# Kernel optimization log

Hardware: AMD Instinct MI355X
Metric: run time of the kernel (lower is better)

Reference implementation:

```python
import jax, jax.numpy as jnp
import numpy as np

H = 256          # HIDDEN_SIZE
OUT = 3          # output_size (hard-coded SOS input width in the torch code)
N_TO_PREDICT = 64
B, S = 256, 512  # batch, encoder sequence length
IN = H + OUT     # LSTM input size = hidden*D + output_size


def setup_inputs() -> dict:
    key = jax.random.key(0)
    ks = jax.random.split(key, 16)
    sc = 0.05
    return {
        "encoder_outputs": jax.random.normal(ks[0], (B, S, H), jnp.float32),
        "encoder_hidden": jax.random.normal(ks[1], (1, B, H), jnp.float32),
        "encoder_cell": jax.random.normal(ks[2], (1, B, H), jnp.float32),
        # attention params (Va is defined in the torch module but unused in forward)
        "Wa": jax.random.normal(ks[3], (H, H), jnp.float32) * sc,
        "ba": jax.random.normal(ks[4], (H,), jnp.float32) * sc,
        "Ua": jax.random.normal(ks[5], (H, H), jnp.float32) * sc,
        "bua": jax.random.normal(ks[6], (H,), jnp.float32) * sc,
        # single-layer unidirectional LSTM params (torch gate order i,f,g,o)
        "W_ih": jax.random.normal(ks[7], (4 * H, IN), jnp.float32) * sc,
        "W_hh": jax.random.normal(ks[8], (4 * H, H), jnp.float32) * sc,
        "b_ih": jax.random.normal(ks[9], (4 * H,), jnp.float32) * sc,
        "b_hh": jax.random.normal(ks[10], (4 * H,), jnp.float32) * sc,
        # output projection
        "Wo": jax.random.normal(ks[11], (OUT, H), jnp.float32) * sc,
        "bo": jax.random.normal(ks[12], (OUT,), jnp.float32) * sc,
    }


def reference(encoder_outputs, encoder_hidden, encoder_cell,
              Wa, ba, Ua, bua, W_ih, W_hh, b_ih, b_hh, Wo, bo):
    # Precompute Ua(keys): [B,S,H] (same math as recomputing it each step)
    UK = jnp.einsum('bsh,gh->bsg', encoder_outputs, Ua) + bua
    h0 = encoder_hidden[0]  # [B,H] (num_layers=1, unidirectional)
    c0 = encoder_cell[0]
    x0 = jnp.zeros((encoder_outputs.shape[0], OUT), encoder_outputs.dtype)  # SOS_token = 0

    def step(carry, _):
        h, c, x_in = carry
        # Bahdanau-style score as written: Ua(keys) . Wa(query)
        wq = h @ Wa.T + ba                                   # [B,H]
        scores = jnp.einsum('bsh,bh->bs', UK, wq)            # [B,S]
        w = jax.nn.softmax(scores, axis=-1)                  # [B,S]
        ctx = jnp.einsum('bs,bsh->bh', w, encoder_outputs)   # [B,H]
        x = jnp.concatenate([x_in, ctx], axis=-1)            # [B, OUT+H]
        gates = x @ W_ih.T + b_ih + h @ W_hh.T + b_hh        # [B,4H]
        i, f, g, o = jnp.split(gates, 4, axis=-1)
        c_new = jax.nn.sigmoid(f) * c + jax.nn.sigmoid(i) * jnp.tanh(g)
        h_new = jax.nn.sigmoid(o) * jnp.tanh(c_new)
        pred = h_new @ Wo.T + bo                             # [B,OUT]
        return (h_new, c_new, jax.lax.stop_gradient(pred)), (pred, w)

    (hN, cN, _), (preds, attns) = jax.lax.scan(step, (h0, c0, x0), None, length=N_TO_PREDICT)
    predictions = jnp.transpose(preds, (1, 0, 2))   # [B, N, OUT]
    attentions = jnp.transpose(attns, (1, 0, 2))    # [B, N, S]
    decoder_hidden = hN[None]                        # [1, B, H]
    return predictions, decoder_hidden, attentions
```

## Files before the change

kernel.cpp:

```cpp
#include <hip/hip_runtime.h>
#include <math.h>

#define HID   256
#define SEQ   512
#define BATCH 256
#define NPRED 64
#define NOUT  3
#define KP2   264
#define GATES 1024

typedef unsigned int u32;
typedef _Float16 half2_t __attribute__((ext_vector_type(2)));
typedef __fp16   fp16x2_t __attribute__((ext_vector_type(2)));

__device__ __forceinline__ float sigmoidf_(float x) { return 1.0f / (1.0f + __expf(-x)); }
__device__ __forceinline__ float tanhf_(float x)    { return 1.0f - 2.0f / (__expf(2.0f * x) + 1.0f); }

__device__ __forceinline__ float fdot2_(u32 a, u32 b, float c) {
#if __has_builtin(__builtin_amdgcn_fdot2)
    union { u32 u; half2_t h; } x, y; x.u = a; y.u = b;
    return __builtin_amdgcn_fdot2(x.h, y.h, c, false);
#else
    union { u32 u; _Float16 h[2]; } x, y; x.u = a; y.u = b;
    return c + (float)x.h[0] * (float)y.h[0] + (float)x.h[1] * (float)y.h[1];
#endif
}
__device__ __forceinline__ u32 pkrtz_(float a, float b) {
#if __has_builtin(__builtin_amdgcn_cvt_pkrtz)
    union { fp16x2_t h; u32 u; } c; c.h = __builtin_amdgcn_cvt_pkrtz(a, b); return c.u;
#else
    union { _Float16 h[2]; u32 u; } c; c.h[0] = (_Float16)a; c.h[1] = (_Float16)b; return c.u;
#endif
}
__device__ __forceinline__ u32 pkrne_(float a, float b) {
    union { _Float16 h[2]; u32 u; } c; c.h[0] = (_Float16)a; c.h[1] = (_Float16)b; return c.u;
}
__device__ __forceinline__ u32 pkfma_(u32 a, u32 b, u32 c) {
    union { u32 u; half2_t h; } x, y, z, r; x.u = a; y.u = b; z.u = c;
    r.h = x.h * y.h + z.h;
    return r.u;
}
__device__ __forceinline__ u32 pkadd_(u32 a, u32 b) {
    union { u32 u; half2_t h; } x, y, r; x.u = a; y.u = b;
    r.h = x.h + y.h;
    return r.u;
}
__device__ __forceinline__ float lof_(u32 u) {
    union { u32 x; half2_t h; } c; c.x = u; return (float)c.h[0];
}
__device__ __forceinline__ float hif_(u32 u) {
    union { u32 x; half2_t h; } c; c.x = u; return (float)c.h[1];
}

__device__ __forceinline__ float colval_(const float* W_ih, const float* W_hh, int g, int k) {
    if (k < 3)   return W_ih[g * 259 + k];
    if (k == 3)  return 0.f;
    if (k < 260) return W_ih[g * 259 + (k - 1)];
    if (k < 516) return W_hh[g * HID + (k - 260)];
    return 0.f;
}
__global__ void prep_wc(const float* __restrict__ W_ih,
                        const float* __restrict__ W_hh,
                        uint4* __restrict__ Wc2) {
    const int p = blockIdx.x;
    const int j = threadIdx.x;
    u32 comp[4];
    #pragma unroll
    for (int q = 0; q < 4; ++q) {
        const int g = 4 * j + q;
        comp[q] = pkrne_(colval_(W_ih, W_hh, g, 2 * p),
                         colval_(W_ih, W_hh, g, 2 * p + 1));
    }
    Wc2[p * 256 + j] = make_uint4(comp[0], comp[1], comp[2], comp[3]);
}

__global__ void prep_ma(const float* __restrict__ Wa,
                        const float* __restrict__ Ua,
                        uint2* __restrict__ Ma2) {
    const int k4 = blockIdx.x;
    const int j  = threadIdx.x;
    float acc[4] = {0.f, 0.f, 0.f, 0.f};
    for (int m = 0; m < HID; ++m) {
        const float ua = Ua[m * HID + j];
        #pragma unroll
        for (int q = 0; q < 4; ++q)
            acc[q] += Wa[m * HID + 4 * k4 + q] * ua;
    }
    Ma2[k4 * 256 + j] = make_uint2(pkrne_(acc[0], acc[1]), pkrne_(acc[2], acc[3]));
}

__global__ void prep_misc(const float* __restrict__ b_ih,
                          const float* __restrict__ b_hh,
                          const float* __restrict__ ba,
                          const float* __restrict__ Ua,
                          float* __restrict__ bias_g,
                          float* __restrict__ v0) {
    const int t = threadIdx.x;
    if (t < GATES) bias_g[t] = b_ih[t] + b_hh[t];
    if (t < HID) {
        float acc = 0.f;
        for (int m = 0; m < HID; ++m) acc += ba[m] * Ua[m * HID + t];
        v0[t] = acc;
    }
}

__device__ __forceinline__ void p1_body(const uint2* __restrict__ Ma2,
                                        const float* __restrict__ v0,
                                        const u32* s_xh, u32* s_vqh, int j) {
    float a0 = 0.f, a1 = 0.f;
    #pragma unroll 8
    for (int p2 = 0; p2 < 64; ++p2) {
        const uint2 ma = Ma2[(p2 << 8) + j];
        const uint2 hh = *(const uint2*)&s_xh[130 + (p2 << 1)];
        a0 = fdot2_(ma.x, hh.x, a0);
        a1 = fdot2_(ma.y, hh.y, a1);
    }
    float acc = v0[j] + a0 + a1;
    const float accN = __shfl_xor(acc, 1);
    if (!(j & 1)) s_vqh[j >> 1] = pkrtz_(acc, accN);
}

__global__ __launch_bounds__(1024)
void decoder_kernel(const float* __restrict__ enc,
                    const float* __restrict__ h0,
                    const float* __restrict__ c0,
                    const float* __restrict__ Wo,
                    const float* __restrict__ bo,
                    const uint2* __restrict__ Ma2,
                    const float* __restrict__ v0,
                    const uint4* __restrict__ Wc2,
                    const float* __restrict__ bias_g,
                    float* __restrict__ pred_out,
                    float* __restrict__ hid_out,
                    float* __restrict__ attn_out)
{
    const int b    = blockIdx.x;
    const int t    = threadIdx.x;
    const int wave = t >> 6;
    const int lane = t & 63;
    const int rg   = t >> 4;
    const int hc   = t & 15;

    __shared__ __align__(16) float s_h[HID], s_c[HID];
    __shared__ __align__(16) u32   s_vqh[HID / 2];
    __shared__ __align__(16) u32   s_xh[KP2];
    __shared__ __align__(16) float s_gp[4096];
    __shared__ __align__(16) float s_wmax[16], s_wsum[16], s_pred[4];
    u32* const s_gpu = (u32*)s_gp;

    u32 encR[64];
    {
        const float* ep = enc + ((size_t)b * SEQ + rg * 8) * HID + hc * 16;
        #pragma unroll
        for (int rr = 0; rr < 8; ++rr) {
            #pragma unroll
            for (int i2 = 0; i2 < 4; ++i2) {
                const float4 f = *(const float4*)(ep + rr * HID + i2 * 4);
                encR[rr * 8 + i2 * 2]     = pkrne_(f.x, f.y);
                encR[rr * 8 + i2 * 2 + 1] = pkrne_(f.z, f.w);
            }
        }
    }

    if (t < HID) {
        const float hv = h0[b * HID + t];
        s_h[t] = hv;
        s_c[t] = c0[b * HID + t];
        const float hN = __shfl_xor(hv, 1);
        if (!(t & 1)) s_xh[130 + (t >> 1)] = pkrtz_(hv, hN);
    }
    if (t < 2) s_xh[t] = 0u;
    if (t >= 258 && t < KP2) s_xh[t] = 0u;
    if (t < 4) s_pred[t] = 0.f;
    __syncthreads();

    if (t >= 256 && t < 512) p1_body(Ma2, v0, s_xh, s_vqh, t & 255);
    __syncthreads();

    for (int n = 0; n < NPRED; ++n) {
        float acc[8];
        {
            u32 vq[8];
            *(uint4*)&vq[0] = *(const uint4*)&s_vqh[hc * 8];
            *(uint4*)&vq[4] = *(const uint4*)&s_vqh[hc * 8 + 4];
            #pragma unroll
            for (int rr = 0; rr < 8; ++rr) {
                float a = 0.f;
                #pragma unroll
                for (int i = 0; i < 8; ++i) a = fdot2_(encR[rr * 8 + i], vq[i], a);
                acc[rr] = a;
            }
        }
        #pragma unroll
        for (int rr = 0; rr < 8; ++rr) {
            acc[rr] += __shfl_xor(acc[rr], 1);
            acc[rr] += __shfl_xor(acc[rr], 2);
            acc[rr] += __shfl_xor(acc[rr], 4);
            acc[rr] += __shfl_xor(acc[rr], 8);
        }
        float mx = acc[0];
        #pragma unroll
        for (int rr = 1; rr < 8; ++rr) mx = fmaxf(mx, acc[rr]);
        mx = fmaxf(mx, __shfl_xor(mx, 16));
        mx = fmaxf(mx, __shfl_xor(mx, 32));
        if (lane == 0) s_wmax[wave] = mx;
        __syncthreads();

        float M;
        {
            const float4* q4 = (const float4*)s_wmax;
            float4 v = q4[0];
            M = fmaxf(fmaxf(v.x, v.y), fmaxf(v.z, v.w));
            #pragma unroll
            for (int w = 1; w < 4; ++w) {
                v = q4[w];
                M = fmaxf(M, fmaxf(fmaxf(v.x, v.y), fmaxf(v.z, v.w)));
            }
        }
        float e[8];
        #pragma unroll
        for (int rr = 0; rr < 8; ++rr) e[rr] = __expf(acc[rr] - M);
        float su = e[0];
        #pragma unroll
        for (int rr = 1; rr < 8; ++rr) su += e[rr];
        su += __shfl_xor(su, 16);
        su += __shfl_xor(su, 32);
        if (lane == 0) s_wsum[wave] = su;
        __syncthreads();

        float L = 0.f;
        {
            const float4* q4 = (const float4*)s_wsum;
            #pragma unroll
            for (int w = 0; w < 4; ++w) {
                const float4 v = q4[w];
                L += (v.x + v.y) + (v.z + v.w);
            }
        }
        const float invL = 1.0f / L;
        if (hc == 0) {
            float* ap = attn_out + ((size_t)b * NPRED + n) * SEQ + rg * 8;
            float4 o0, o1;
            o0.x = e[0] * invL; o0.y = e[1] * invL; o0.z = e[2] * invL; o0.w = e[3] * invL;
            o1.x = e[4] * invL; o1.y = e[5] * invL; o1.z = e[6] * invL; o1.w = e[7] * invL;
            *(float4*)ap = o0; *(float4*)(ap + 4) = o1;
        }
        u32 wp[8];
        #pragma unroll
        for (int rr = 0; rr < 8; ++rr) {
            const float wn = e[rr] * invL;
            wp[rr] = pkrne_(wn, wn);
        }
        u32 ah[8];
        #pragma unroll
        for (int i = 0; i < 8; ++i) ah[i] = 0u;
        #pragma unroll
        for (int rr = 0; rr < 8; ++rr) {
            #pragma unroll
            for (int i = 0; i < 8; ++i)
                ah[i] = pkfma_(encR[rr * 8 + i], wp[rr], ah[i]);
        }
        #pragma unroll
        for (int i = 0; i < 8; ++i) {
            u32 v = ah[i];
            v = pkadd_(v, (u32)__shfl_xor((int)v, 16));
            v = pkadd_(v, (u32)__shfl_xor((int)v, 32));
            ah[i] = v;
        }
        if ((lane >> 4) == 0) {
            *(uint4*)&s_gpu[wave * 128 + hc * 8]     = *(const uint4*)&ah[0];
            *(uint4*)&s_gpu[wave * 128 + hc * 8 + 4] = *(const uint4*)&ah[4];
        }
        __syncthreads();

        if (t < 128) {
            float cx = 0.f, cy = 0.f;
            #pragma unroll
            for (int w = 0; w < 16; ++w) {
                const u32 u = s_gpu[w * 128 + t];
                cx += lof_(u);
                cy += hif_(u);
            }
            s_xh[2 + t] = pkrne_(cx, cy);
        }
        if (t == 256) {
            s_xh[0] = pkrtz_(s_pred[0], s_pred[1]);
            s_xh[1] = pkrtz_(s_pred[2], 0.f);
        }
        __syncthreads();

        {
            const int j  = t & 255;
            const int ks = t >> 8;
            float4 g4 = {0.f, 0.f, 0.f, 0.f};
            const int pbeg = ks * 66;
            #pragma unroll 3
            for (int pp = 0; pp < 66; ++pp) {
                const int p = pbeg + pp;
                const uint4 w = Wc2[(p << 8) + j];
                const u32 x = s_xh[p];
                g4.x = fdot2_(w.x, x, g4.x);
                g4.y = fdot2_(w.y, x, g4.y);
                g4.z = fdot2_(w.z, x, g4.z);
                g4.w = fdot2_(w.w, x, g4.w);
            }
            *(float4*)&s_gp[(ks << 10) + (j << 2)] = g4;
        }
        __syncthreads();

        if (t < HID) {
            float gv[4];
            #pragma unroll
            for (int q = 0; q < 4; ++q) {
                const int gi = (q << 8) + t;
                gv[q] = bias_g[gi] + s_gp[gi] + s_gp[1024 + gi]
                      + s_gp[2048 + gi] + s_gp[3072 + gi];
            }
            const float cn = sigmoidf_(gv[1]) * s_c[t] + sigmoidf_(gv[0]) * tanhf_(gv[2]);
            const float hn = sigmoidf_(gv[3]) * tanhf_(cn);
            s_c[t] = cn;
            s_h[t] = hn;
            const float hN = __shfl_xor(hn, 1);
            if (!(t & 1)) s_xh[130 + (t >> 1)] = pkrtz_(hn, hN);
        }
        __syncthreads();

        if (wave < NOUT) {
            const float4 w4 = *(const float4*)&Wo[wave * HID + (lane << 2)];
            const float4 h4 = *(const float4*)&s_h[lane << 2];
            float p = w4.x * h4.x + w4.y * h4.y + w4.z * h4.z + w4.w * h4.w;
            #pragma unroll
            for (int off = 32; off >= 1; off >>= 1) p += __shfl_xor(p, off);
            if (lane == 0) {
                p += bo[wave];
                s_pred[wave] = p;
                pred_out[((size_t)b * NPRED + n) * NOUT + wave] = p;
            }
        } else if (t >= 256 && t < 512 && n + 1 < NPRED) {
            p1_body(Ma2, v0, s_xh, s_vqh, t & 255);
        }
        __syncthreads();
    }

    if (t < HID) hid_out[b * HID + t] = s_h[t];
}

extern "C" void kernel_launch(void* const* d_in, const int* in_sizes, int n_in,
                              void* d_out, int out_size, void* d_ws, size_t ws_size,
                              hipStream_t stream) {
    const float* enc  = (const float*)d_in[0];
    const float* h0   = (const float*)d_in[1];
    const float* c0   = (const float*)d_in[2];
    const float* Wa   = (const float*)d_in[3];
    const float* ba   = (const float*)d_in[4];
    const float* Ua   = (const float*)d_in[5];
    const float* W_ih = (const float*)d_in[7];
    const float* W_hh = (const float*)d_in[8];
    const float* b_ih = (const float*)d_in[9];
    const float* b_hh = (const float*)d_in[10];
    const float* Wo   = (const float*)d_in[11];
    const float* bo   = (const float*)d_in[12];

    char* ws = (char*)d_ws;
    uint4* Wc2    = (uint4*)ws;                      ws += (size_t)KP2 * 256 * 16;
    uint2* Ma2    = (uint2*)ws;                      ws += (size_t)64 * 256 * 8;
    float* v0     = (float*)ws;                      ws += 256 * 4;
    float* bias_g = (float*)ws;                      ws += GATES * 4;
    (void)ws_size;

    float* pred_out = (float*)d_out;
    float* hid_out  = pred_out + BATCH * NPRED * NOUT;
    float* attn_out = hid_out + BATCH * HID;

    prep_wc  <<<dim3(KP2), dim3(256),  0, stream>>>(W_ih, W_hh, Wc2);
    prep_ma  <<<dim3(64),  dim3(256),  0, stream>>>(Wa, Ua, Ma2);
    prep_misc<<<dim3(1),   dim3(1024), 0, stream>>>(b_ih, b_hh, ba, Ua, bias_g, v0);
    decoder_kernel<<<dim3(BATCH), dim3(1024), 0, stream>>>(
        enc, h0, c0, Wo, bo, Ma2, v0, Wc2, bias_g,
        pred_out, hid_out, attn_out);
}
```

Before: 1.415 ms.

## Overlap hidden-state gate matvec with prediction phase and defer softmax normalization

```diff
diff --git a/kernel.cpp b/kernel.cpp
--- a/kernel.cpp
+++ b/kernel.cpp
@@ -108,7 +108,7 @@
                                         const float* __restrict__ v0,
                                         const u32* s_xh, u32* s_vqh, int j) {
     float a0 = 0.f, a1 = 0.f;
-    #pragma unroll 8
+    #pragma unroll 16
     for (int p2 = 0; p2 < 64; ++p2) {
         const uint2 ma = Ma2[(p2 << 8) + j];
         const uint2 hh = *(const uint2*)&s_xh[130 + (p2 << 1)];
@@ -118,6 +118,24 @@
     float acc = v0[j] + a0 + a1;
     const float accN = __shfl_xor(acc, 1);
     if (!(j & 1)) s_vqh[j >> 1] = pkrtz_(acc, accN);
+}
+
+__device__ __forceinline__ void eh_body(const uint4* __restrict__ Wc2,
+                                        const u32* s_xh, float* s_gp,
+                                        int j, int ks2) {
+    float4 g4 = {0.f, 0.f, 0.f, 0.f};
+    const int pbeg = 130 + ks2 * 67;
+    #pragma unroll
+    for (int pp = 0; pp < 67; ++pp) {
+        const int p = pbeg + pp;
+        const uint4 w = Wc2[(p << 8) + j];
+        const u32 x = s_xh[p];
+        g4.x = fdot2_(w.x, x, g4.x);
+        g4.y = fdot2_(w.y, x, g4.y);
+        g4.z = fdot2_(w.z, x, g4.z);
+        g4.w = fdot2_(w.w, x, g4.w);
+    }
+    *(float4*)&s_gp[((4 + ks2) << 10) + (j << 2)] = g4;
 }
 
 __global__ __launch_bounds__(1024)
@@ -144,7 +162,7 @@
     __shared__ __align__(16) float s_h[HID], s_c[HID];
     __shared__ __align__(16) u32   s_vqh[HID / 2];
     __shared__ __align__(16) u32   s_xh[KP2];
-    __shared__ __align__(16) float s_gp[4096];
+    __shared__ __align__(16) float s_gp[6144];
     __shared__ __align__(16) float s_wmax[16], s_wsum[16], s_pred[4];
     u32* const s_gpu = (u32*)s_gp;
 
@@ -174,7 +192,8 @@
     if (t < 4) s_pred[t] = 0.f;
     __syncthreads();
 
-    if (t >= 256 && t < 512) p1_body(Ma2, v0, s_xh, s_vqh, t & 255);
+    if (wave >= 4 && wave < 8)      p1_body(Ma2, v0, s_xh, s_vqh, t & 255);
+    else if (wave >= 8)             eh_body(Wc2, s_xh, s_gp, t & 255, (t >> 8) - 2);
     __syncthreads();
 
     for (int n = 0; n < NPRED; ++n) {
@@ -226,6 +245,30 @@
         su += __shfl_xor(su, 16);
         su += __shfl_xor(su, 32);
         if (lane == 0) s_wsum[wave] = su;
+
+        {
+            u32 ah[8];
+            #pragma unroll
+            for (int i = 0; i < 8; ++i) ah[i] = 0u;
+            #pragma unroll
+            for (int rr = 0; rr < 8; ++rr) {
+                const u32 wp = pkrne_(e[rr], e[rr]);
+                #pragma unroll
+                for (int i = 0; i < 8; ++i)
+                    ah[i] = pkfma_(encR[rr * 8 + i], wp, ah[i]);
+            }
+            #pragma unroll
+            for (int i = 0; i < 8; ++i) {
+                u32 v = ah[i];
+                v = pkadd_(v, (u32)__shfl_xor((int)v, 16));
+                v = pkadd_(v, (u32)__shfl_xor((int)v, 32));
+                ah[i] = v;
+            }
+            if ((lane >> 4) == 0) {
+                *(uint4*)&s_gpu[wave * 128 + hc * 8]     = *(const uint4*)&ah[0];
+                *(uint4*)&s_gpu[wave * 128 + hc * 8 + 4] = *(const uint4*)&ah[4];
+            }
+        }
         __syncthreads();
 
         float L = 0.f;
@@ -238,6 +281,16 @@
             }
         }
         const float invL = 1.0f / L;
+        if (t < 128) {
+            float cx = 0.f, cy = 0.f;
+            #pragma unroll
+            for (int w = 0; w < 16; ++w) {
+                const u32 u = s_gpu[w * 128 + t];
+                cx += lof_(u);
+                cy += hif_(u);
+            }
+            s_xh[2 + t] = pkrne_(cx * invL, cy * invL);
+        }
         if (hc == 0) {
             float* ap = attn_out + ((size_t)b * NPRED + n) * SEQ + rg * 8;
             float4 o0, o1;
@@ -245,44 +298,6 @@
             o1.x = e[4] * invL; o1.y = e[5] * invL; o1.z = e[6] * invL; o1.w = e[7] * invL;
             *(float4*)ap = o0; *(float4*)(ap + 4) = o1;
         }
-        u32 wp[8];
-        #pragma unroll
-        for (int rr = 0; rr < 8; ++rr) {
-            const float wn = e[rr] * invL;
-            wp[rr] = pkrne_(wn, wn);
-        }
-        u32 ah[8];
-        #pragma unroll
-        for (int i = 0; i < 8; ++i) ah[i] = 0u;
-        #pragma unroll
-        for (int rr = 0; rr < 8; ++rr) {
-            #pragma unroll
-            for (int i = 0; i < 8; ++i)
-                ah[i] = pkfma_(encR[rr * 8 + i], wp[rr], ah[i]);
-        }
-        #pragma unroll
-        for (int i = 0; i < 8; ++i) {
-            u32 v = ah[i];
-            v = pkadd_(v, (u32)__shfl_xor((int)v, 16));
-            v = pkadd_(v, (u32)__shfl_xor((int)v, 32));
-            ah[i] = v;
-        }
-        if ((lane >> 4) == 0) {
-            *(uint4*)&s_gpu[wave * 128 + hc * 8]     = *(const uint4*)&ah[0];
-            *(uint4*)&s_gpu[wave * 128 + hc * 8 + 4] = *(const uint4*)&ah[4];
-        }
-        __syncthreads();
-
-        if (t < 128) {
-            float cx = 0.f, cy = 0.f;
-            #pragma unroll
-            for (int w = 0; w < 16; ++w) {
-                const u32 u = s_gpu[w * 128 + t];
-                cx += lof_(u);
-                cy += hif_(u);
-            }
-            s_xh[2 + t] = pkrne_(cx, cy);
-        }
         if (t == 256) {
             s_xh[0] = pkrtz_(s_pred[0], s_pred[1]);
             s_xh[1] = pkrtz_(s_pred[2], 0.f);
@@ -292,17 +307,20 @@
         {
             const int j  = t & 255;
             const int ks = t >> 8;
+            const int pbeg = (ks < 2) ? 33 * ks : 66 + 32 * (ks - 2);
+            const int cnt  = (ks < 2) ? 33 : 32;
             float4 g4 = {0.f, 0.f, 0.f, 0.f};
-            const int pbeg = ks * 66;
-            #pragma unroll 3
-            for (int pp = 0; pp < 66; ++pp) {
-                const int p = pbeg + pp;
-                const uint4 w = Wc2[(p << 8) + j];
-                const u32 x = s_xh[p];
-                g4.x = fdot2_(w.x, x, g4.x);
-                g4.y = fdot2_(w.y, x, g4.y);
-                g4.z = fdot2_(w.z, x, g4.z);
-                g4.w = fdot2_(w.w, x, g4.w);
+            #pragma unroll
+            for (int pp = 0; pp < 33; ++pp) {
+                if (pp < cnt) {
+                    const int p = pbeg + pp;
+                    const uint4 w = Wc2[(p << 8) + j];
+                    const u32 x = s_xh[p];
+                    g4.x = fdot2_(w.x, x, g4.x);
+                    g4.y = fdot2_(w.y, x, g4.y);
+                    g4.z = fdot2_(w.z, x, g4.z);
+                    g4.w = fdot2_(w.w, x, g4.w);
+                }
             }
             *(float4*)&s_gp[(ks << 10) + (j << 2)] = g4;
         }
@@ -314,7 +332,8 @@
             for (int q = 0; q < 4; ++q) {
                 const int gi = (q << 8) + t;
                 gv[q] = bias_g[gi] + s_gp[gi] + s_gp[1024 + gi]
-                      + s_gp[2048 + gi] + s_gp[3072 + gi];
+                      + s_gp[2048 + gi] + s_gp[3072 + gi]
+                      + s_gp[4096 + gi] + s_gp[5120 + gi];
             }
             const float cn = sigmoidf_(gv[1]) * s_c[t] + sigmoidf_(gv[0]) * tanhf_(gv[2]);
             const float hn = sigmoidf_(gv[3]) * tanhf_(cn);
@@ -336,8 +355,10 @@
                 s_pred[wave] = p;
                 pred_out[((size_t)b * NPRED + n) * NOUT + wave] = p;
             }
-        } else if (t >= 256 && t < 512 && n + 1 < NPRED) {
-            p1_body(Ma2, v0, s_xh, s_vqh, t & 255);
+        } else if (wave >= 4 && wave < 8) {
+            if (n + 1 < NPRED) p1_body(Ma2, v0, s_xh, s_vqh, t & 255);
+        } else if (wave >= 8) {
+            if (n + 1 < NPRED) eh_body(Wc2, s_xh, s_gp, t & 255, (t >> 8) - 2);
         }
         __syncthreads();
     }
```

Result: slower. 5.486 ms (+287.7%).
